# Optimization experiments

Hardware: AMD Instinct MI355X
Metric: run time of the kernel (lower is better)

## Reference

```python
import jax, jax.numpy as jnp
import numpy as np

D_MODEL = 512
PROJ = 2 * D_MODEL  # 1024
N_STATES = 32
KSIZE = 4
LN_EPS = 1e-3  # keras LayerNormalization default epsilon


def setup_inputs() -> dict:
    key = jax.random.key(0)
    ks = jax.random.split(key, 16)
    B, L = 2, 2048
    s_in = 1.0 / np.sqrt(D_MODEL)
    s_pr = 1.0 / np.sqrt(PROJ)
    x = jax.random.normal(ks[0], (B, L, D_MODEL), dtype=jnp.float32)
    # LayerNorm params
    ln_gamma = jnp.ones((D_MODEL,), jnp.float32)
    ln_beta = jnp.zeros((D_MODEL,), jnp.float32)
    # dense1 / dense2: d_model -> proj
    W1 = jax.random.normal(ks[1], (D_MODEL, PROJ), jnp.float32) * s_in
    b1 = jnp.zeros((PROJ,), jnp.float32)
    W2 = jax.random.normal(ks[2], (D_MODEL, PROJ), jnp.float32) * s_in
    b2 = jnp.zeros((PROJ,), jnp.float32)
    # depthwise causal conv1d: kernel (K, 1, PROJ) in WIO layout, groups=PROJ
    conv_k = jax.random.normal(ks[3], (KSIZE, 1, PROJ), jnp.float32) * 0.5
    conv_b = jnp.zeros((PROJ,), jnp.float32)
    # SSM params
    A_log = jnp.log(jnp.broadcast_to(jnp.arange(1, N_STATES + 1, dtype=jnp.float32), (PROJ, N_STATES)))
    D_skip = jnp.ones((PROJ,), jnp.float32)
    WB = jax.random.normal(ks[4], (PROJ, N_STATES), jnp.float32) * s_pr
    bB = jnp.zeros((N_STATES,), jnp.float32)
    WC = jax.random.normal(ks[5], (PROJ, N_STATES), jnp.float32) * s_pr
    bC = jnp.zeros((N_STATES,), jnp.float32)
    Wd = jax.random.normal(ks[6], (PROJ, PROJ), jnp.float32) * s_pr
    bd = jnp.zeros((PROJ,), jnp.float32)
    # dense3: proj -> d_model
    W3 = jax.random.normal(ks[7], (PROJ, D_MODEL), jnp.float32) * s_pr
    b3 = jnp.zeros((D_MODEL,), jnp.float32)
    return dict(x=x, ln_gamma=ln_gamma, ln_beta=ln_beta, W1=W1, b1=b1, W2=W2, b2=b2,
                conv_k=conv_k, conv_b=conv_b, A_log=A_log, D_skip=D_skip,
                WB=WB, bB=bB, WC=WC, bC=bC, Wd=Wd, bd=bd, W3=W3, b3=b3)


def _layernorm(x, gamma, beta):
    mu = jnp.mean(x, axis=-1, keepdims=True)
    var = jnp.mean(jnp.square(x - mu), axis=-1, keepdims=True)
    return (x - mu) * jax.lax.rsqrt(var + LN_EPS) * gamma + beta


def _causal_dwconv(x, k, b):
    # x: [B,L,C], k: [K,1,C], depthwise causal conv (left-pad K-1)
    y = jax.lax.conv_general_dilated(
        x, k, window_strides=(1,), padding=[(KSIZE - 1, 0)],
        dimension_numbers=('NWC', 'WIO', 'NWC'), feature_group_count=PROJ)
    return y + b


def _selective_scan(u, delta, A, Bm, Cm, D_skip):
    # u, delta: [B,L,D]; A: [D,N]; Bm, Cm: [B,L,N]; D_skip: [D]
    deltaA = jnp.einsum('bld,dn->bldn', delta, A)                 # [B,L,D,N]
    deltaBu = jnp.einsum('bld,bld,bln->bldn', delta, u, Bm)        # [B,L,D,N]
    # shift deltaA left by one along L, zero at the end (pad trick in source)
    shifted = jnp.concatenate([deltaA[:, 1:], jnp.zeros_like(deltaA[:, :1])], axis=1)
    # reversed cumsum along L, then exp
    e = jnp.exp(jnp.flip(jnp.cumsum(jnp.flip(shifted, axis=1), axis=1), axis=1))
    xs = jnp.cumsum(deltaBu * e, axis=1) / (e + 1e-12)
    y = jnp.einsum('bldn,bln->bld', xs, Cm)
    return y + u * D_skip


def reference(x, ln_gamma, ln_beta, W1, b1, W2, b2, conv_k, conv_b,
              A_log, D_skip, WB, bB, WC, bC, Wd, bd, W3, b3):
    h = _layernorm(x, ln_gamma, ln_beta)
    x1 = h @ W1 + b1                      # [B,L,PROJ]
    x1 = _causal_dwconv(x1, conv_k, conv_b)
    x1 = jax.nn.silu(x1)
    A = -jnp.exp(A_log)                    # [PROJ,N]
    Cm = x1 @ WC + bC                      # [B,L,N]
    Bm = x1 @ WB + bB                      # [B,L,N]
    delta = jax.nn.softplus(x1 @ Wd + bd)  # [B,L,PROJ]
    y = _selective_scan(x1, delta, A, Bm, Cm, D_skip)
    x2 = jax.nn.silu(h @ W2 + b2)
    out = (y * x2) @ W3 + b3 + x           # residual; dropout is identity at inference
    return out
```

## Files before the change

kernel.cpp:

```cpp
#include <hip/hip_runtime.h>
#include <stdint.h>

#define L_SEQ 2048
#define BATCH 2
#define DMODEL 512
#define PROJ 1024
#define NST 32
#define NCAT 1152
#define ROWS (BATCH*L_SEQ)
#define THRESH 50.0f

typedef float f32x4 __attribute__((ext_vector_type(4)));
typedef short short8 __attribute__((ext_vector_type(8)));

__device__ inline float bf2f(unsigned short u){ uint32_t x=((uint32_t)u)<<16; float f; __builtin_memcpy(&f,&x,4); return f; }
__device__ inline unsigned short f2bf(float f){ uint32_t x; __builtin_memcpy(&x,&f,4); uint32_t r=x+0x7FFFu+((x>>16)&1u); return (unsigned short)(r>>16); }
__device__ inline float siluf(float x){ return x/(1.f+__expf(-x)); }
__device__ inline float softplusf(float x){ return x>20.f? x : log1pf(__expf(x)); }

#define AS1(p) ((const __attribute__((address_space(1))) void*)(p))
#define AS3(p) ((__attribute__((address_space(3))) void*)(p))

template<int N> __device__ inline void wait_vmcnt(){
  if constexpr (N==0)      asm volatile("s_waitcnt vmcnt(0)" ::: "memory");
  else if constexpr (N==4) asm volatile("s_waitcnt vmcnt(4)" ::: "memory");
  else if constexpr (N==6) asm volatile("s_waitcnt vmcnt(6)" ::: "memory");
  else                     asm volatile("s_waitcnt vmcnt(8)" ::: "memory");
}

__global__ __launch_bounds__(256)
void prep_kernel(const float* __restrict__ W1, const float* __restrict__ b1,
                 const float* __restrict__ W2, const float* __restrict__ b2,
                 const float* __restrict__ Wd, const float* __restrict__ bd,
                 const float* __restrict__ WB, const float* __restrict__ bB,
                 const float* __restrict__ WC, const float* __restrict__ bC,
                 const float* __restrict__ W3,
                 unsigned short* __restrict__ W12t, unsigned short* __restrict__ Wcatt,
                 unsigned short* __restrict__ W3t, float* __restrict__ bias12,
                 float* __restrict__ biascat)
{
  int i = blockIdx.x*256 + threadIdx.x;
  const int nA = 2048*512;
  const int nB = NCAT*1024;
  const int nC = 512*1024;
  if (i < nA) {
    int n = i >> 9, k = i & 511;
    float v = (n < 1024) ? W1[k*1024 + n] : W2[k*1024 + (n-1024)];
    W12t[i] = f2bf(v);
    return;
  }
  i -= nA;
  if (i < nB) {
    int n = i >> 10, k = i & 1023;
    float v;
    if (n < 1024) v = Wd[k*1024 + n];
    else if (n < 1056) v = WB[k*32 + (n-1024)];
    else if (n < 1088) v = WC[k*32 + (n-1056)];
    else v = 0.f;
    Wcatt[i] = f2bf(v);
    return;
  }
  i -= nB;
  if (i < nC) {
    int n = i >> 10, k = i & 1023;
    W3t[i] = f2bf(W3[k*512 + n]);
    return;
  }
  i -= nC;
  if (i < 2048) { bias12[i] = (i < 1024) ? b1[i] : b2[i-1024]; return; }
  i -= 2048;
  if (i < NCAT) {
    biascat[i] = (i < 1024) ? bd[i] : (i < 1056) ? bB[i-1024] : (i < 1088) ? bC[i-1056] : 0.f;
  }
}

__global__ __launch_bounds__(256)
void ln_kernel(const float* __restrict__ x, const float* __restrict__ gamma,
               const float* __restrict__ beta, unsigned short* __restrict__ H)
{
  int row = blockIdx.x*4 + (threadIdx.x >> 6);
  int lane = threadIdx.x & 63;
  const float4* xr = (const float4*)(x + (size_t)row*DMODEL);
  float4 v0 = xr[lane];
  float4 v1 = xr[lane+64];
  float s = v0.x+v0.y+v0.z+v0.w + v1.x+v1.y+v1.z+v1.w;
  float q = v0.x*v0.x+v0.y*v0.y+v0.z*v0.z+v0.w*v0.w
          + v1.x*v1.x+v1.y*v1.y+v1.z*v1.z+v1.w*v1.w;
#pragma unroll
  for (int m=32;m>0;m>>=1){ s += __shfl_xor(s,m); q += __shfl_xor(q,m); }
  float mu = s*(1.f/DMODEL);
  float var = q*(1.f/DMODEL) - mu*mu;
  float rs = rsqrtf(var + 1e-3f);
  int c0 = lane*4, c1 = 256 + lane*4;
  float4 g0 = *(const float4*)&gamma[c0]; float4 g1 = *(const float4*)&gamma[c1];
  float4 t0 = *(const float4*)&beta[c0];  float4 t1 = *(const float4*)&beta[c1];
  ushort4 o0, o1;
  o0.x = f2bf((v0.x-mu)*rs*g0.x + t0.x);
  o0.y = f2bf((v0.y-mu)*rs*g0.y + t0.y);
  o0.z = f2bf((v0.z-mu)*rs*g0.z + t0.z);
  o0.w = f2bf((v0.w-mu)*rs*g0.w + t0.w);
  o1.x = f2bf((v1.x-mu)*rs*g1.x + t1.x);
  o1.y = f2bf((v1.y-mu)*rs*g1.y + t1.y);
  o1.z = f2bf((v1.z-mu)*rs*g1.z + t1.z);
  o1.w = f2bf((v1.w-mu)*rs*g1.w + t1.w);
  *(ushort4*)&H[(size_t)row*DMODEL + c0] = o0;
  *(ushort4*)&H[(size_t)row*DMODEL + c1] = o1;
}

template<int BM, int BN, int MODE>
__global__ __launch_bounds__(256)
void gemm_bt(const unsigned short* __restrict__ A, const unsigned short* __restrict__ Bt,
             void* __restrict__ Cv, const float* __restrict__ bias,
             const float* __restrict__ res, int M, int N, int K)
{
  constexpr int BK = 64;
  constexpr int BMW = BM/2, BNW = BN/2;
  constexpr int AM = BMW/16, AN = BNW/16;
  constexpr int ASEGI = BM/32;
  constexpr int BSEGI = BN/32;
  constexpr int LPT = ASEGI + BSEGI;
  __shared__ unsigned short As[3][BM*BK];
  __shared__ unsigned short Bs[3][BN*BK];
  int tid = threadIdx.x;
  int lane = tid & 63, wid = tid >> 6;
  int wm = wid >> 1, wn = wid & 1;

  int gx = gridDim.x;
  int nwg = gx * gridDim.y;
  int L = blockIdx.y*gx + blockIdx.x;
  int W = (L & 7)*(nwg >> 3) + (L >> 3);
  int bx = W % gx, by = W / gx;
  int m0 = bx*BM, n0 = by*BN;

  f32x4 acc[AM][AN];
#pragma unroll
  for (int i=0;i<AM;i++)
#pragma unroll
    for (int j=0;j<AN;j++)
#pragma unroll
      for (int e=0;e<4;e++) acc[i][j][e] = 0.f;

  const unsigned short* ap[ASEGI];
  const unsigned short* bp[BSEGI];
#pragma unroll
  for (int j=0;j<ASEGI;j++){
    int s = tid + j*256;
    int row = s >> 3, kc = ((s & 7) ^ (row & 7)) * 8;
    ap[j] = A + (size_t)(m0+row)*K + kc;
  }
#pragma unroll
  for (int j=0;j<BSEGI;j++){
    int s = tid + j*256;
    int row = s >> 3, kc = ((s & 7) ^ (row & 7)) * 8;
    bp[j] = Bt + (size_t)(n0+row)*K + kc;
  }

  auto stage = [&](int buf){
#pragma unroll
    for (int j=0;j<ASEGI;j++){
      __builtin_amdgcn_global_load_lds(AS1(ap[j]), AS3(&As[buf][(size_t)(j*256 + wid*64)*8]), 16, 0, 0);
      ap[j] += BK;
    }
#pragma unroll
    for (int j=0;j<BSEGI;j++){
      __builtin_amdgcn_global_load_lds(AS1(bp[j]), AS3(&Bs[buf][(size_t)(j*256 + wid*64)*8]), 16, 0, 0);
      bp[j] += BK;
    }
  };

  stage(0);
  stage(1);
  int T = K/BK;
  int rb = 0, wb = 2;
  int r = lane & 15, kb = lane >> 4;
  for (int t = 0; t < T; ++t) {
    if (t+1 < T) wait_vmcnt<LPT>();
    else         wait_vmcnt<0>();
    __builtin_amdgcn_s_barrier();
    if (t+2 < T) { stage(wb); wb = (wb==2)?0:wb+1; }
#pragma unroll
    for (int ks=0; ks<2; ++ks) {
      int cx = (ks*4 + kb) ^ (r & 7);
      short8 af[AM], bfr[AN];
#pragma unroll
      for (int i=0;i<AM;i++){
        int row = wm*BMW + i*16 + r;
        af[i] = *(const short8*)&As[rb][(row*8 + cx)*8];
      }
#pragma unroll
      for (int j=0;j<AN;j++){
        int row = wn*BNW + j*16 + r;
        bfr[j] = *(const short8*)&Bs[rb][(row*8 + cx)*8];
      }
#pragma unroll
      for (int i=0;i<AM;i++)
#pragma unroll
        for (int j=0;j<AN;j++)
          acc[i][j] = __builtin_amdgcn_mfma_f32_16x16x32_bf16(af[i], bfr[j], acc[i][j], 0,0,0);
    }
    rb = (rb==2)?0:rb+1;
  }

  int rr = (lane >> 4)*4, cc = lane & 15;
#pragma unroll
  for (int i=0;i<AM;i++)
#pragma unroll
    for (int j=0;j<AN;j++) {
      int col = n0 + wn*BNW + j*16 + cc;
      float bcol = (MODE == 2) ? 0.f : bias[col];
#pragma unroll
      for (int e=0;e<4;e++) {
        int row = m0 + wm*BMW + i*16 + rr + e;
        float v = acc[i][j][e];
        if constexpr (MODE == 2) {
          v += bias[row];
          if (row < 1024) v = softplusf(v);
          ((float*)Cv)[(size_t)row*N + col] = v;
        } else if constexpr (MODE == 1) {
          ((unsigned short*)Cv)[(size_t)row*N + col] = f2bf(v + bcol);
        } else {
          v += bcol + res[(size_t)row*N + col];
          ((float*)Cv)[(size_t)row*N + col] = v;
        }
      }
    }
}

__global__ __launch_bounds__(256)
void conv_silu_kernel(const unsigned short* __restrict__ P12, const float* __restrict__ ck,
                      const float* __restrict__ cb, unsigned short* __restrict__ ubf,
                      unsigned short* __restrict__ x2bf)
{
  int gid = blockIdx.x*256 + threadIdx.x;
  int c4 = gid & 511;
  int row = gid >> 9;
  int l = row & (L_SEQ-1);
  if (c4 < 256) {
    int c = c4*4;
    float4 bv = *(const float4*)&cb[c];
    float r0=bv.x, r1=bv.y, r2=bv.z, r3=bv.w;
#pragma unroll
    for (int t=0;t<4;t++){
      int lsrc = l - 3 + t;
      if (lsrc >= 0) {
        ushort4 xv = *(const ushort4*)&P12[(size_t)(row-3+t)*2048 + c];
        float4 kv = *(const float4*)&ck[t*PROJ + c];
        r0 = fmaf(bf2f(xv.x),kv.x,r0);
        r1 = fmaf(bf2f(xv.y),kv.y,r1);
        r2 = fmaf(bf2f(xv.z),kv.z,r2);
        r3 = fmaf(bf2f(xv.w),kv.w,r3);
      }
    }
    ushort4 o;
    o.x=f2bf(siluf(r0)); o.y=f2bf(siluf(r1)); o.z=f2bf(siluf(r2)); o.w=f2bf(siluf(r3));
    *(ushort4*)&ubf[(size_t)row*PROJ + c] = o;
  } else {
    int c = (c4-256)*4;
    ushort4 xv = *(const ushort4*)&P12[(size_t)row*2048 + 1024 + c];
    ushort4 o;
    o.x=f2bf(siluf(bf2f(xv.x))); o.y=f2bf(siluf(bf2f(xv.y)));
    o.z=f2bf(siluf(bf2f(xv.z))); o.w=f2bf(siluf(bf2f(xv.w)));
    *(ushort4*)&x2bf[(size_t)row*PROJ + c] = o;
  }
}

__global__ __launch_bounds__(256)
void sscan_kernel(const float* __restrict__ CT, const unsigned short* __restrict__ ubf,
                  const float* __restrict__ A_log, int* __restrict__ l0out,
                  unsigned short* __restrict__ ystate)
{
  __shared__ float suf8sh[8][256];
  int tid = threadIdx.x;
  int n = tid & 31, gsub = tid >> 5;
  int G = blockIdx.x*8 + gsub;
  int b = G >> 10, d = G & 1023;
  const float* dT = CT + (size_t)d*ROWS + b*L_SEQ;

  float mysum = 0.f;
  {
    const float4* c4 = (const float4*)(dT + n*64);
    for (int it=0; it<16; ++it){ float4 v = c4[it]; mysum += v.x+v.y+v.z+v.w; }
  }
  float incl = mysum;
#pragma unroll
  for (int dlt=1; dlt<32; dlt<<=1){ float t = __shfl_up(incl, dlt, 32); if (n >= dlt) incl += t; }
  float Tot = __shfl(incl, 31, 32);
  float excl = incl - mysum;
  int cnt = 0;
  {
    const float4* c4 = (const float4*)(dT + n*64);
    float run = excl;
    for (int it=0; it<16; ++it){
      float4 v = c4[it];
      if ((it & 1) == 0) suf8sh[gsub][n*8 + (it>>1)] = Tot - run;
      cnt += (Tot - run >= THRESH); run += v.x;
      cnt += (Tot - run >= THRESH); run += v.y;
      cnt += (Tot - run >= THRESH); run += v.z;
      cnt += (Tot - run >= THRESH); run += v.w;
    }
  }
#pragma unroll
  for (int m=16;m>0;m>>=1) cnt += __shfl_xor(cnt, m, 32);
  int myl0 = cnt > 0 ? cnt-1 : 0;
  if (n == 0) l0out[G] = myl0;
  __syncthreads();

  int base = min(myl0, __shfl_xor(myl0, 32)) & ~7;
  float np1 = __expf(A_log[d*NST + n]);
  const float* Br = CT + (size_t)(1024+n)*ROWS + b*L_SEQ;
  const float* Cr = CT + (size_t)(1056+n)*ROWS + b*L_SEQ;
  const unsigned short* ub = ubf + (size_t)b*L_SEQ*PROJ + d;
  unsigned short* yb = ystate + (size_t)b*L_SEQ*PROJ + d;
  float s = 0.f;
  for (int l = base; l < L_SEQ; l += 8) {
    float4 d0 = *(const float4*)&dT[l];
    float4 d1 = *(const float4*)&dT[l+4];
    float4 B0 = *(const float4*)&Br[l];
    float4 B1 = *(const float4*)&Br[l+4];
    float4 C0 = *(const float4*)&Cr[l];
    float4 C1 = *(const float4*)&Cr[l+4];
    float sufv = suf8sh[gsub][l >> 3];
    float dl[8] = {d0.x,d0.y,d0.z,d0.w,d1.x,d1.y,d1.z,d1.w};
    float Bv[8] = {B0.x,B0.y,B0.z,B0.w,B1.x,B1.y,B1.z,B1.w};
    float Cv[8] = {C0.x,C0.y,C0.z,C0.w,C1.x,C1.y,C1.z,C1.w};
    float uu[8];
#pragma unroll
    for (int t=0;t<8;t++) uu[t] = bf2f(ub[(size_t)(l+t)*PROJ]);
    float cum = 0.f;
#pragma unroll
    for (int t=0;t<8;t++){
      cum += dl[t];
      float decay = __expf(-dl[t]*np1);
      s = fmaf(decay, s, dl[t]*uu[t]*Bv[t]);
      float gte = 1.f/(1.f + 1e-12f*__expf(np1*(sufv - cum)));
      float contrib = s*gte*Cv[t];
#pragma unroll
      for (int m=16;m>0;m>>=1) contrib += __shfl_xor(contrib, m);
      if (n == 0) yb[(size_t)(l+t)*PROJ] = f2bf(contrib);
    }
  }
}

__global__ __launch_bounds__(256)
void zmul_kernel(const unsigned short* __restrict__ ystate, const unsigned short* __restrict__ ubf,
                 const unsigned short* __restrict__ x2bf, const float* __restrict__ Dskip,
                 const int* __restrict__ l0arr, unsigned short* __restrict__ zbf)
{
  size_t i = ((size_t)blockIdx.x*256 + threadIdx.x)*4;
  int d = (int)(i & (PROJ-1));
  int row = (int)(i >> 10);
  int l = row & (L_SEQ-1);
  int b = row >> 11;
  int4 l0v = *(const int4*)&l0arr[b*PROJ + d];
  ushort4 yu = *(const ushort4*)&ystate[i];
  float ysx = (l >= l0v.x) ? bf2f(yu.x) : 0.f;
  float ysy = (l >= l0v.y) ? bf2f(yu.y) : 0.f;
  float ysz = (l >= l0v.z) ? bf2f(yu.z) : 0.f;
  float ysw = (l >= l0v.w) ? bf2f(yu.w) : 0.f;
  ushort4 uu = *(const ushort4*)&ubf[i];
  ushort4 xx = *(const ushort4*)&x2bf[i];
  float4 Dv = *(const float4*)&Dskip[d];
  ushort4 o;
  o.x = f2bf((ysx + bf2f(uu.x)*Dv.x)*bf2f(xx.x));
  o.y = f2bf((ysy + bf2f(uu.y)*Dv.y)*bf2f(xx.y));
  o.z = f2bf((ysz + bf2f(uu.z)*Dv.z)*bf2f(xx.z));
  o.w = f2bf((ysw + bf2f(uu.w)*Dv.w)*bf2f(xx.w));
  *(ushort4*)&zbf[i] = o;
}

extern "C" void kernel_launch(void* const* d_in, const int* in_sizes, int n_in,
                              void* d_out, int out_size, void* d_ws, size_t ws_size,
                              hipStream_t stream)
{
  const float* x     = (const float*)d_in[0];
  const float* ln_g  = (const float*)d_in[1];
  const float* ln_b  = (const float*)d_in[2];
  const float* W1    = (const float*)d_in[3];
  const float* b1    = (const float*)d_in[4];
  const float* W2    = (const float*)d_in[5];
  const float* b2    = (const float*)d_in[6];
  const float* convk = (const float*)d_in[7];
  const float* convb = (const float*)d_in[8];
  const float* A_log = (const float*)d_in[9];
  const float* Dskip = (const float*)d_in[10];
  const float* WB    = (const float*)d_in[11];
  const float* bB    = (const float*)d_in[12];
  const float* WC    = (const float*)d_in[13];
  const float* bC    = (const float*)d_in[14];
  const float* Wd    = (const float*)d_in[15];
  const float* bd    = (const float*)d_in[16];
  const float* W3    = (const float*)d_in[17];
  const float* b3    = (const float*)d_in[18];

  char* w = (char*)d_ws;
  auto alloc = [&](size_t bytes){ char* p = w; w += (bytes + 255) & ~(size_t)255; return p; };
  unsigned short* Hbf    = (unsigned short*)alloc((size_t)ROWS*DMODEL*2);
  unsigned short* W12t   = (unsigned short*)alloc((size_t)2048*512*2);
  unsigned short* Wcatt  = (unsigned short*)alloc((size_t)NCAT*1024*2);
  unsigned short* W3t    = (unsigned short*)alloc((size_t)512*1024*2);
  float*          bias12 = (float*)alloc(2048*4);
  float*          biascat= (float*)alloc(NCAT*4);
  unsigned short* P12    = (unsigned short*)alloc((size_t)ROWS*2048*2);
  unsigned short* ubf    = (unsigned short*)alloc((size_t)ROWS*PROJ*2);
  unsigned short* x2bf   = (unsigned short*)alloc((size_t)ROWS*PROJ*2);
  float*          CT     = (float*)alloc((size_t)NCAT*ROWS*4);
  int*            l0arr  = (int*)alloc(2048*4);
  unsigned short* ystate = (unsigned short*)alloc((size_t)ROWS*PROJ*2);
  unsigned short* zbf    = (unsigned short*)alloc((size_t)ROWS*PROJ*2);

  {
    int total = 2048*512 + NCAT*1024 + 512*1024 + 2048 + NCAT;
    prep_kernel<<<(total+255)/256, 256, 0, stream>>>(W1,b1,W2,b2,Wd,bd,WB,bB,WC,bC,W3,
                                                     W12t,Wcatt,W3t,bias12,biascat);
  }
  ln_kernel<<<ROWS/4, 256, 0, stream>>>(x, ln_g, ln_b, Hbf);

  dim3 g1(ROWS/128, 2048/64);
  gemm_bt<128,64,1><<<g1, 256, 0, stream>>>(Hbf, W12t, P12, bias12, nullptr, ROWS, 2048, DMODEL);

  conv_silu_kernel<<<ROWS*512/256, 256, 0, stream>>>(P12, convk, convb, ubf, x2bf);

  dim3 g2(NCAT/128, ROWS/64);
  gemm_bt<128,64,2><<<g2, 256, 0, stream>>>(Wcatt, ubf, CT, biascat, nullptr, NCAT, ROWS, PROJ);

  sscan_kernel<<<2048/8, 256, 0, stream>>>(CT, ubf, A_log, l0arr, ystate);

  zmul_kernel<<<(ROWS*PROJ/4)/256, 256, 0, stream>>>(ystate, ubf, x2bf, Dskip, l0arr, zbf);

  dim3 g3(ROWS/128, DMODEL/64);
  gemm_bt<128,64,3><<<g3, 256, 0, stream>>>(zbf, W3t, (float*)d_out, b3, x, ROWS, DMODEL, PROJ);
}
```

Before: 166.3 us.

## Use 64x64 GEMM tiles, split-K final GEMM, trim padded columns, tiled weight transpose

```diff
diff --git a/kernel.cpp b/kernel.cpp
--- a/kernel.cpp
+++ b/kernel.cpp
@@ -6,7 +6,7 @@
 #define DMODEL 512
 #define PROJ 1024
 #define NST 32
-#define NCAT 1152
+#define NCATU 1088
 #define ROWS (BATCH*L_SEQ)
 #define THRESH 50.0f
 
@@ -24,7 +24,6 @@
 template<int N> __device__ inline void wait_vmcnt(){
   if constexpr (N==0)      asm volatile("s_waitcnt vmcnt(0)" ::: "memory");
   else if constexpr (N==4) asm volatile("s_waitcnt vmcnt(4)" ::: "memory");
-  else if constexpr (N==6) asm volatile("s_waitcnt vmcnt(6)" ::: "memory");
   else                     asm volatile("s_waitcnt vmcnt(8)" ::: "memory");
 }
 
@@ -39,39 +38,59 @@
                  unsigned short* __restrict__ W3t, float* __restrict__ bias12,
                  float* __restrict__ biascat)
 {
-  int i = blockIdx.x*256 + threadIdx.x;
-  const int nA = 2048*512;
-  const int nB = NCAT*1024;
-  const int nC = 512*1024;
-  if (i < nA) {
-    int n = i >> 9, k = i & 511;
-    float v = (n < 1024) ? W1[k*1024 + n] : W2[k*1024 + (n-1024)];
-    W12t[i] = f2bf(v);
+  __shared__ float tile[32][33];
+  int bid = blockIdx.x;
+  int lx = threadIdx.x & 31, ly = threadIdx.x >> 5;
+  if (bid < 1024) {
+    int kt = bid & 15, nt = bid >> 4;
+    int k0 = kt*32, n0 = nt*32;
+    const float* S = (n0 < 1024) ? W1 : W2;
+    int nc = (n0 < 1024) ? n0 : n0 - 1024;
+#pragma unroll
+    for (int i=0;i<4;i++)
+      tile[ly+i*8][lx] = S[(size_t)(k0+ly+i*8)*1024 + nc + lx];
+    __syncthreads();
+#pragma unroll
+    for (int i=0;i<4;i++)
+      W12t[(size_t)(n0+ly+i*8)*512 + k0 + lx] = f2bf(tile[lx][ly+i*8]);
     return;
   }
-  i -= nA;
-  if (i < nB) {
-    int n = i >> 10, k = i & 1023;
-    float v;
-    if (n < 1024) v = Wd[k*1024 + n];
-    else if (n < 1056) v = WB[k*32 + (n-1024)];
-    else if (n < 1088) v = WC[k*32 + (n-1056)];
-    else v = 0.f;
-    Wcatt[i] = f2bf(v);
+  if (bid < 2112) {
+    int t = bid - 1024;
+    int kt = t & 31, nt = t >> 5;
+    int k0 = kt*32, n0 = nt*32;
+#pragma unroll
+    for (int i=0;i<4;i++){
+      int k = k0 + ly + i*8;
+      float v;
+      if (n0 < 1024)       v = Wd[(size_t)k*1024 + n0 + lx];
+      else if (n0 == 1024) v = WB[(size_t)k*32 + lx];
+      else                 v = WC[(size_t)k*32 + lx];
+      tile[ly+i*8][lx] = v;
+    }
+    __syncthreads();
+#pragma unroll
+    for (int i=0;i<4;i++)
+      Wcatt[(size_t)(n0+ly+i*8)*1024 + k0 + lx] = f2bf(tile[lx][ly+i*8]);
     return;
   }
-  i -= nB;
-  if (i < nC) {
-    int n = i >> 10, k = i & 1023;
-    W3t[i] = f2bf(W3[k*512 + n]);
+  if (bid < 2624) {
+    int t = bid - 2112;
+    int kt = t & 31, nt = t >> 5;
+    int k0 = kt*32, n0 = nt*32;
+#pragma unroll
+    for (int i=0;i<4;i++)
+      tile[ly+i*8][lx] = W3[(size_t)(k0+ly+i*8)*512 + n0 + lx];
+    __syncthreads();
+#pragma unroll
+    for (int i=0;i<4;i++)
+      W3t[(size_t)(n0+ly+i*8)*1024 + k0 + lx] = f2bf(tile[lx][ly+i*8]);
     return;
   }
-  i -= nC;
-  if (i < 2048) { bias12[i] = (i < 1024) ? b1[i] : b2[i-1024]; return; }
-  i -= 2048;
-  if (i < NCAT) {
-    biascat[i] = (i < 1024) ? bd[i] : (i < 1056) ? bB[i-1024] : (i < 1088) ? bC[i-1056] : 0.f;
-  }
+  int j = (bid - 2624)*256 + threadIdx.x;
+  if (j < 2048) { bias12[j] = (j < 1024) ? b1[j] : b2[j-1024]; return; }
+  j -= 2048;
+  if (j < NCATU) biascat[j] = (j < 1024) ? bd[j] : (j < 1056) ? bB[j-1024] : bC[j-1056];
 }
 
 __global__ __launch_bounds__(256)
@@ -107,20 +126,16 @@
   *(ushort4*)&H[(size_t)row*DMODEL + c1] = o1;
 }
 
-template<int BM, int BN, int MODE>
+template<int MODE>
 __global__ __launch_bounds__(256)
 void gemm_bt(const unsigned short* __restrict__ A, const unsigned short* __restrict__ Bt,
              void* __restrict__ Cv, const float* __restrict__ bias,
-             const float* __restrict__ res, int M, int N, int K)
+             const float* __restrict__ res, int M, int N, int K, int Kfull)
 {
   constexpr int BK = 64;
-  constexpr int BMW = BM/2, BNW = BN/2;
-  constexpr int AM = BMW/16, AN = BNW/16;
-  constexpr int ASEGI = BM/32;
-  constexpr int BSEGI = BN/32;
-  constexpr int LPT = ASEGI + BSEGI;
-  __shared__ unsigned short As[3][BM*BK];
-  __shared__ unsigned short Bs[3][BN*BK];
+  constexpr int LPT = 4;
+  __shared__ unsigned short As[3][64*BK];
+  __shared__ unsigned short Bs[3][64*BK];
   int tid = threadIdx.x;
   int lane = tid & 63, wid = tid >> 6;
   int wm = wid >> 1, wn = wid & 1;
@@ -130,39 +145,35 @@
   int L = blockIdx.y*gx + blockIdx.x;
   int W = (L & 7)*(nwg >> 3) + (L >> 3);
   int bx = W % gx, by = W / gx;
-  int m0 = bx*BM, n0 = by*BN;
-
-  f32x4 acc[AM][AN];
-#pragma unroll
-  for (int i=0;i<AM;i++)
-#pragma unroll
-    for (int j=0;j<AN;j++)
+  int m0 = bx*64, n0 = by*64;
+  int kofs = blockIdx.z*K;
+
+  f32x4 acc[2][2];
+#pragma unroll
+  for (int i=0;i<2;i++)
+#pragma unroll
+    for (int j=0;j<2;j++)
 #pragma unroll
       for (int e=0;e<4;e++) acc[i][j][e] = 0.f;
 
-  const unsigned short* ap[ASEGI];
-  const unsigned short* bp[BSEGI];
-#pragma unroll
-  for (int j=0;j<ASEGI;j++){
+  const unsigned short* ap[2];
+  const unsigned short* bp[2];
+#pragma unroll
+  for (int j=0;j<2;j++){
     int s = tid + j*256;
     int row = s >> 3, kc = ((s & 7) ^ (row & 7)) * 8;
-    ap[j] = A + (size_t)(m0+row)*K + kc;
-  }
-#pragma unroll
-  for (int j=0;j<BSEGI;j++){
-    int s = tid + j*256;
-    int row = s >> 3, kc = ((s & 7) ^ (row & 7)) * 8;
-    bp[j] = Bt + (size_t)(n0+row)*K + kc;
+    ap[j] = A + (size_t)(m0+row)*Kfull + kofs + kc;
+    bp[j] = Bt + (size_t)(n0+row)*Kfull + kofs + kc;
   }
 
   auto stage = [&](int buf){
 #pragma unroll
-    for (int j=0;j<ASEGI;j++){
+    for (int j=0;j<2;j++){
       __builtin_amdgcn_global_load_lds(AS1(ap[j]), AS3(&As[buf][(size_t)(j*256 + wid*64)*8]), 16, 0, 0);
       ap[j] += BK;
     }
 #pragma unroll
-    for (int j=0;j<BSEGI;j++){
+    for (int j=0;j<2;j++){
       __builtin_amdgcn_global_load_lds(AS1(bp[j]), AS3(&Bs[buf][(size_t)(j*256 + wid*64)*8]), 16, 0, 0);
       bp[j] += BK;
     }
@@ -181,36 +192,38 @@
 #pragma unroll
     for (int ks=0; ks<2; ++ks) {
       int cx = (ks*4 + kb) ^ (r & 7);
-      short8 af[AM], bfr[AN];
-#pragma unroll
-      for (int i=0;i<AM;i++){
-        int row = wm*BMW + i*16 + r;
+      short8 af[2], bfr[2];
+#pragma unroll
+      for (int i=0;i<2;i++){
+        int row = wm*32 + i*16 + r;
         af[i] = *(const short8*)&As[rb][(row*8 + cx)*8];
       }
 #pragma unroll
-      for (int j=0;j<AN;j++){
-        int row = wn*BNW + j*16 + r;
+      for (int j=0;j<2;j++){
+        int row = wn*32 + j*16 + r;
         bfr[j] = *(const short8*)&Bs[rb][(row*8 + cx)*8];
       }
-#pragma unroll
-      for (int i=0;i<AM;i++)
-#pragma unroll
-        for (int j=0;j<AN;j++)
+      __builtin_amdgcn_s_setprio(1);
+#pragma unroll
+      for (int i=0;i<2;i++)
+#pragma unroll
+        for (int j=0;j<2;j++)
           acc[i][j] = __builtin_amdgcn_mfma_f32_16x16x32_bf16(af[i], bfr[j], acc[i][j], 0,0,0);
+      __builtin_amdgcn_s_setprio(0);
     }
     rb = (rb==2)?0:rb+1;
   }
 
   int rr = (lane >> 4)*4, cc = lane & 15;
 #pragma unroll
-  for (int i=0;i<AM;i++)
-#pragma unroll
-    for (int j=0;j<AN;j++) {
-      int col = n0 + wn*BNW + j*16 + cc;
-      float bcol = (MODE == 2) ? 0.f : bias[col];
+  for (int i=0;i<2;i++)
+#pragma unroll
+    for (int j=0;j<2;j++) {
+      int col = n0 + wn*32 + j*16 + cc;
+      float bcol = (MODE == 1) ? bias[col] : 0.f;
 #pragma unroll
       for (int e=0;e<4;e++) {
-        int row = m0 + wm*BMW + i*16 + rr + e;
+        int row = m0 + wm*32 + i*16 + rr + e;
         float v = acc[i][j][e];
         if constexpr (MODE == 2) {
           v += bias[row];
@@ -219,11 +232,28 @@
         } else if constexpr (MODE == 1) {
           ((unsigned short*)Cv)[(size_t)row*N + col] = f2bf(v + bcol);
         } else {
-          v += bcol + res[(size_t)row*N + col];
-          ((float*)Cv)[(size_t)row*N + col] = v;
+          ((float*)Cv)[(size_t)blockIdx.z*M*N + (size_t)row*N + col] = v;
         }
       }
     }
+}
+
+__global__ __launch_bounds__(256)
+void reduce_kernel(const float* __restrict__ P, const float* __restrict__ x,
+                   const float* __restrict__ b3, float* __restrict__ out)
+{
+  size_t i = ((size_t)blockIdx.x*256 + threadIdx.x)*4;
+  int col = (int)(i & 511);
+  float4 a = *(const float4*)&P[i];
+  float4 b = *(const float4*)&P[(size_t)ROWS*512 + i];
+  float4 xv = *(const float4*)&x[i];
+  float4 bv = *(const float4*)&b3[col];
+  float4 o;
+  o.x = a.x + b.x + xv.x + bv.x;
+  o.y = a.y + b.y + xv.y + bv.y;
+  o.z = a.z + b.z + xv.z + bv.z;
+  o.w = a.w + b.w + xv.w + bv.w;
+  *(float4*)&out[i] = o;
 }
 
 __global__ __launch_bounds__(256)
@@ -396,37 +426,36 @@
   auto alloc = [&](size_t bytes){ char* p = w; w += (bytes + 255) & ~(size_t)255; return p; };
   unsigned short* Hbf    = (unsigned short*)alloc((size_t)ROWS*DMODEL*2);
   unsigned short* W12t   = (unsigned short*)alloc((size_t)2048*512*2);
-  unsigned short* Wcatt  = (unsigned short*)alloc((size_t)NCAT*1024*2);
+  unsigned short* Wcatt  = (unsigned short*)alloc((size_t)NCATU*1024*2);
   unsigned short* W3t    = (unsigned short*)alloc((size_t)512*1024*2);
   float*          bias12 = (float*)alloc(2048*4);
-  float*          biascat= (float*)alloc(NCAT*4);
+  float*          biascat= (float*)alloc(NCATU*4);
   unsigned short* P12    = (unsigned short*)alloc((size_t)ROWS*2048*2);
   unsigned short* ubf    = (unsigned short*)alloc((size_t)ROWS*PROJ*2);
   unsigned short* x2bf   = (unsigned short*)alloc((size_t)ROWS*PROJ*2);
-  float*          CT     = (float*)alloc((size_t)NCAT*ROWS*4);
+  float*          CT     = (float*)alloc((size_t)NCATU*ROWS*4);
   int*            l0arr  = (int*)alloc(2048*4);
   unsigned short* ystate = (unsigned short*)alloc((size_t)ROWS*PROJ*2);
   unsigned short* zbf    = (unsigned short*)alloc((size_t)ROWS*PROJ*2);
-
-  {
-    int total = 2048*512 + NCAT*1024 + 512*1024 + 2048 + NCAT;
-    prep_kernel<<<(total+255)/256, 256, 0, stream>>>(W1,b1,W2,b2,Wd,bd,WB,bB,WC,bC,W3,
-                                                     W12t,Wcatt,W3t,bias12,biascat);
-  }
+  float*          Pp     = (float*)alloc((size_t)2*ROWS*512*4);
+
+  prep_kernel<<<2637, 256, 0, stream>>>(W1,b1,W2,b2,Wd,bd,WB,bB,WC,bC,W3,
+                                        W12t,Wcatt,W3t,bias12,biascat);
   ln_kernel<<<ROWS/4, 256, 0, stream>>>(x, ln_g, ln_b, Hbf);
 
-  dim3 g1(ROWS/128, 2048/64);
-  gemm_bt<128,64,1><<<g1, 256, 0, stream>>>(Hbf, W12t, P12, bias12, nullptr, ROWS, 2048, DMODEL);
+  dim3 g1(ROWS/64, 2048/64);
+  gemm_bt<1><<<g1, 256, 0, stream>>>(Hbf, W12t, P12, bias12, nullptr, ROWS, 2048, DMODEL, DMODEL);
 
   conv_silu_kernel<<<ROWS*512/256, 256, 0, stream>>>(P12, convk, convb, ubf, x2bf);
 
-  dim3 g2(NCAT/128, ROWS/64);
-  gemm_bt<128,64,2><<<g2, 256, 0, stream>>>(Wcatt, ubf, CT, biascat, nullptr, NCAT, ROWS, PROJ);
+  dim3 g2(NCATU/64, ROWS/64);
+  gemm_bt<2><<<g2, 256, 0, stream>>>(Wcatt, ubf, CT, biascat, nullptr, NCATU, ROWS, PROJ, PROJ);
 
   sscan_kernel<<<2048/8, 256, 0, stream>>>(CT, ubf, A_log, l0arr, ystate);
 
   zmul_kernel<<<(ROWS*PROJ/4)/256, 256, 0, stream>>>(ystate, ubf, x2bf, Dskip, l0arr, zbf);
 
-  dim3 g3(ROWS/128, DMODEL/64);
-  gemm_bt<128,64,3><<<g3, 256, 0, stream>>>(zbf, W3t, (float*)d_out, b3, x, ROWS, DMODEL, PROJ);
-}
+  dim3 g3(ROWS/64, 512/64, 2);
+  gemm_bt<5><<<g3, 256, 0, stream>>>(zbf, W3t, Pp, b3, nullptr, ROWS, 512, 512, PROJ);
+  reduce_kernel<<<(ROWS*512/4)/256, 256, 0, stream>>>(Pp, x, b3, (float*)d_out);
+}
```

New measurement: 160.0 us. 3.8% less time.
